# Kernel tuning notes

Measured on AMD Instinct MI355X. Metric: run time of the kernel, lower is better.

## Reference

```python
import jax, jax.numpy as jnp
import numpy as np

N_NODES = 50000
N_EDGES = 1_600_000
IN_DIM = 128
OUT_DIM = 32
HEADS = 4
EDGE_DIM = 16


def setup_inputs() -> dict:
    key = jax.random.key(0)
    ks = jax.random.split(key, 8)
    x = jax.random.normal(ks[0], (N_NODES, IN_DIM), dtype=jnp.float32)
    edge_index = jax.random.randint(ks[1], (2, N_EDGES), 0, N_NODES, dtype=jnp.int32)
    edge_attr = jax.random.normal(ks[2], (N_EDGES, EDGE_DIM), dtype=jnp.float32)
    # parameters (xavier-ish small scale)
    W_lin = jax.random.normal(ks[3], (OUT_DIM * HEADS, IN_DIM), dtype=jnp.float32) * 0.08
    att_src = jax.random.normal(ks[4], (HEADS, OUT_DIM), dtype=jnp.float32) * 0.1
    att_dst = jax.random.normal(ks[5], (HEADS, OUT_DIM), dtype=jnp.float32) * 0.1
    bias = jnp.zeros((OUT_DIM,), dtype=jnp.float32)
    W_edge = jax.random.normal(ks[6], (HEADS, EDGE_DIM), dtype=jnp.float32) * 0.2
    return {"x": x, "edge_index": edge_index, "edge_attr": edge_attr,
            "W_lin": W_lin, "att_src": att_src, "att_dst": att_dst,
            "bias": bias, "W_edge": W_edge}


def reference(x, edge_index, edge_attr, W_lin, att_src, att_dst, bias, W_edge):
    num_nodes = x.shape[0]
    heads, out_dim = att_src.shape
    # h = lin(x) -> [N, H, D]
    h = (x @ W_lin.T).reshape(num_nodes, heads, out_dim)
    # per-node attention terms [N, H]
    a_src = jnp.einsum("nhd,hd->nh", h, att_src)
    a_dst = jnp.einsum("nhd,hd->nh", h, att_dst)
    src, dst = edge_index[0], edge_index[1]
    # edge logits [E, H]
    logits = a_src[src] + a_dst[dst] + edge_attr @ W_edge.T
    logits = jax.nn.leaky_relu(logits, negative_slope=0.2)
    # segment softmax over edges grouped by dst (vectorized across heads)
    max_vals = jax.ops.segment_max(logits, dst, num_segments=num_nodes)  # [N, H]
    exp_s = jnp.exp(logits - max_vals[dst])
    denom = jax.ops.segment_sum(exp_s, dst, num_segments=num_nodes)  # [N, H]
    alpha = exp_s / (denom[dst] + 1e-16)  # [E, H]
    # weighted aggregation: sum_e h[src_e] * alpha_e into dst nodes
    out = h[src] * alpha[:, :, None]  # [E, H, D]
    agg = jax.ops.segment_sum(out, dst, num_segments=num_nodes)  # [N, H, D]
    return agg.mean(axis=1) + bias
```

## Files before the change

kernel.cpp:

```cpp
#include <hip/hip_runtime.h>
#include <hip/hip_fp16.h>

#define N_NODES 50000
#define N_EDGES 1600000
#define IN_DIM  128
#define OUT_DIM 32
#define HEADS   4
#define EDGE_DIM 16

#define NB   512
#define DPB  98
#define CAP  4096
#define SC_CHUNK 2048
#define SC_THREADS 512
#define SC_EPT   4

__global__ __launch_bounds__(256) void k_gemm(
    const float* __restrict__ x, const float* __restrict__ Wl,
    const float* __restrict__ att_src, const float* __restrict__ att_dst,
    __half* __restrict__ h2t, float* __restrict__ a_src,
    float* __restrict__ a_dst) {
  __shared__ float Wt[IN_DIM][68];
  __shared__ float xs[32][132];
  __shared__ float attS[IN_DIM], attD[IN_DIM];
  __shared__ float sred_s[32][4], sred_d[32][4];
  const int t = threadIdx.x;
  const int n0 = blockIdx.x * 32;

  if (t < IN_DIM) { attS[t] = att_src[t]; attD[t] = att_dst[t]; }

  for (int it = 0; it < 16; ++it) {
    int idx = it * 256 + t;
    int node = idx >> 7, i = idx & 127;
    int n = n0 + node;
    xs[node][i] = (n < N_NODES) ? x[(size_t)n * IN_DIM + i] : 0.f;
  }

  const int tx = t & 15, ty = t >> 4;
  const int na = n0 + 2 * ty, nb = na + 1;

  for (int p = 0; p < 2; ++p) {
    __syncthreads();
    for (int it = 0; it < 32; ++it) {
      int idx = it * 256 + t;
      int kg = (idx >> 7) + p * 64, i = idx & 127;
      Wt[i][kg - p * 64] = Wl[(size_t)kg * IN_DIM + i];
    }
    __syncthreads();

    float4 acc0 = {0.f,0.f,0.f,0.f}, acc1 = {0.f,0.f,0.f,0.f};
    for (int i4 = 0; i4 < IN_DIM; i4 += 4) {
      float4 xa = *(const float4*)&xs[2*ty][i4];
      float4 xb = *(const float4*)&xs[2*ty+1][i4];
      const float* xap = (const float*)&xa;
      const float* xbp = (const float*)&xb;
      #pragma unroll
      for (int ii = 0; ii < 4; ++ii) {
        float4 wv = *(const float4*)&Wt[i4+ii][tx*4];
        float a = xap[ii], b = xbp[ii];
        acc0.x += a*wv.x; acc0.y += a*wv.y; acc0.z += a*wv.z; acc0.w += a*wv.w;
        acc1.x += b*wv.x; acc1.y += b*wv.y; acc1.z += b*wv.z; acc1.w += b*wv.w;
      }
    }
    const int k = p*64 + tx*4;
    const int hd = k >> 5, d0 = k & 31;
    const float* ap = (const float*)&acc0;
    const float* bp = (const float*)&acc1;

    float sa = ap[0]*attS[k] + ap[1]*attS[k+1] + ap[2]*attS[k+2] + ap[3]*attS[k+3];
    float da = ap[0]*attD[k] + ap[1]*attD[k+1] + ap[2]*attD[k+2] + ap[3]*attD[k+3];
    float sb = bp[0]*attS[k] + bp[1]*attS[k+1] + bp[2]*attS[k+2] + bp[3]*attS[k+3];
    float db = bp[0]*attD[k] + bp[1]*attD[k+1] + bp[2]*attD[k+2] + bp[3]*attD[k+3];
    #pragma unroll
    for (int off = 1; off <= 4; off <<= 1) {
      sa += __shfl_xor(sa, off); da += __shfl_xor(da, off);
      sb += __shfl_xor(sb, off); db += __shfl_xor(db, off);
    }
    if ((tx & 7) == 0) {
      sred_s[2*ty][hd] = sa; sred_s[2*ty+1][hd] = sb;
      sred_d[2*ty][hd] = da; sred_d[2*ty+1][hd] = db;
    }

    if (na < N_NODES) {
      #pragma unroll
      for (int j = 0; j < 4; ++j)
        h2t[(size_t)na*IN_DIM + (d0+j)*4 + hd] = __float2half(ap[j]);
    }
    if (nb < N_NODES) {
      #pragma unroll
      for (int j = 0; j < 4; ++j)
        h2t[(size_t)nb*IN_DIM + (d0+j)*4 + hd] = __float2half(bp[j]);
    }
  }
  __syncthreads();
  if (t < 128) {
    int node = t >> 2;
    if (n0 + node < N_NODES)
      a_src[(size_t)(n0 + node) * 4 + (t & 3)] = sred_s[node][t & 3];
  } else {
    int tt = t - 128, node = tt >> 2;
    if (n0 + node < N_NODES)
      a_dst[(size_t)(n0 + node) * 4 + (tt & 3)] = sred_d[node][tt & 3];
  }
}

__global__ __launch_bounds__(SC_THREADS) void k_scatter2(
    const int* __restrict__ ei, const float* __restrict__ eattr,
    const float* __restrict__ a_src, const float* __restrict__ a_dst,
    const float* __restrict__ W_edge, unsigned int* __restrict__ gcursor,
    float4* __restrict__ rec, unsigned char* __restrict__ rdl) {
  __shared__ float We[HEADS * EDGE_DIM];
  __shared__ unsigned int cntb[NB], offb[NB];
  __shared__ float4 stg[SC_CHUNK];
  const int t = threadIdx.x;
  if (t < HEADS * EDGE_DIM) We[t] = W_edge[t];
  for (int i = t; i < NB; i += SC_THREADS) cntb[i] = 0u;
  __syncthreads();

  const int base = blockIdx.x * SC_CHUNK;
  unsigned int rx[SC_EPT], ry[SC_EPT], rz[SC_EPT], rw[SC_EPT], rk[SC_EPT];
  int bk[SC_EPT]; bool ok[SC_EPT];

  #pragma unroll
  for (int i = 0; i < SC_EPT; ++i) {
    int e = base + i * SC_THREADS + t;
    ok[i] = (e < N_EDGES);
    if (ok[i]) {
      int src = ei[e], dst = ei[N_EDGES + e];
      float asp[4], adp[4], ea[EDGE_DIM];
      *(float4*)asp = *(const float4*)(a_src + (size_t)src * 4);
      *(float4*)adp = *(const float4*)(a_dst + (size_t)dst * 4);
      #pragma unroll
      for (int j = 0; j < 4; ++j)
        *(float4*)&ea[j*4] = *(const float4*)(eattr + (size_t)e * EDGE_DIM + j*4);
      float pv[HEADS];
      #pragma unroll
      for (int hh = 0; hh < HEADS; ++hh) {
        float sum = asp[hh] + adp[hh];
        #pragma unroll
        for (int j = 0; j < EDGE_DIM; ++j) sum += ea[j] * We[hh*EDGE_DIM + j];
        float lg = (sum > 0.f) ? sum : 0.2f * sum;
        pv[hh] = __expf(lg);
      }
      __half2 p01 = __floats2half2_rn(pv[0], pv[1]);
      __half2 p23 = __floats2half2_rn(pv[2], pv[3]);
      int b = dst / DPB;
      bk[i] = b;
      rx[i] = *(const unsigned int*)&p01;
      ry[i] = *(const unsigned int*)&p23;
      rz[i] = (unsigned int)src;
      rw[i] = (unsigned int)(dst - b * DPB);
      rk[i] = atomicAdd(&cntb[b], 1u);
    }
  }
  __syncthreads();

  if (t < 64) {
    int carry = 0;
    for (int seg = 0; seg < 8; ++seg) {
      int v = (int)cntb[seg * 64 + t];
      int inc = v;
      #pragma unroll
      for (int off = 1; off < 64; off <<= 1) {
        int u = __shfl_up(inc, off);
        if (t >= off) inc += u;
      }
      offb[seg * 64 + t] = (unsigned int)(carry + inc - v);
      carry += __shfl(inc, 63);
    }
  }
  __syncthreads();

  #pragma unroll
  for (int i = 0; i < SC_EPT; ++i) {
    if (ok[i]) {
      float4 r;
      r.x = __uint_as_float(rx[i]); r.y = __uint_as_float(ry[i]);
      r.z = __uint_as_float(rz[i]); r.w = __uint_as_float(rw[i]);
      stg[offb[bk[i]] + rk[i]] = r;
    }
  }
  __syncthreads();

  {
    unsigned int c = cntb[t];
    if (c) {
      unsigned int gb = atomicAdd(&gcursor[t], c);
      unsigned int lo = offb[t];
      float4* dstp = rec + (size_t)t * CAP + gb;
      unsigned char* dl8 = rdl + (size_t)t * CAP + gb;
      for (unsigned int r = 0; r < c; ++r) {
        float4 v = stg[lo + r];
        dstp[r] = v;
        dl8[r] = (unsigned char)__float_as_uint(v.w);
      }
    }
  }
}

__global__ __launch_bounds__(1024) void k_bagg(
    const unsigned int* __restrict__ gcursor, const float4* __restrict__ rec,
    const unsigned char* __restrict__ rdl, const __half* __restrict__ h2t,
    const float* __restrict__ bias, float* __restrict__ out) {
  __shared__ unsigned short idx[CAP];
  __shared__ unsigned int cnt[DPB], off[DPB], cnt2[DPB];
  const int t = threadIdx.x;
  const int b = blockIdx.x;
  const size_t base = (size_t)b * CAP;
  const unsigned int cntT = gcursor[b];

  for (int i = t; i < DPB; i += 1024) { cnt[i] = 0u; cnt2[i] = 0u; }
  __syncthreads();

  for (unsigned int j = t; j < cntT; j += 1024)
    atomicAdd(&cnt[rdl[base + j]], 1u);
  __syncthreads();
  if (t == 0) {
    unsigned int run = 0;
    for (int i = 0; i < DPB; ++i) { off[i] = run; run += cnt[i]; }
  }
  __syncthreads();
  for (unsigned int j = t; j < cntT; j += 1024) {
    int dl = rdl[base + j];
    unsigned int r = atomicAdd(&cnt2[dl], 1u);
    idx[off[dl] + r] = (unsigned short)j;
  }
  __syncthreads();

  const int wv = t >> 6, lane = t & 63, half_ = lane >> 5, dd = lane & 31;
  for (int dl = wv; dl < DPB; dl += 16) {
    int node = b * DPB + dl;
    if (node >= N_NODES) break;
    const unsigned int s0 = off[dl], c = cnt[dl];

    float acc0 = 0.f, acc1 = 0.f, acc2 = 0.f, acc3 = 0.f;
    float dn0 = 0.f, dn1 = 0.f, dn2 = 0.f, dn3 = 0.f;

    unsigned int j = half_;
    for (; j + 2 < c; j += 4) {
      float4 ra = rec[base + idx[s0 + j]];
      float4 rb = rec[base + idx[s0 + j + 2]];
      unsigned int a01 = __float_as_uint(ra.x), a23 = __float_as_uint(ra.y);
      unsigned int b01 = __float_as_uint(rb.x), b23 = __float_as_uint(rb.y);
      int sa = (int)__float_as_uint(ra.z), sb = (int)__float_as_uint(rb.z);
      uint2 hra = *(const uint2*)(h2t + (size_t)sa * IN_DIM + dd * 4);
      uint2 hrb = *(const uint2*)(h2t + (size_t)sb * IN_DIM + dd * 4);
      float2 pa01 = __half22float2(*(const __half2*)&a01);
      float2 pa23 = __half22float2(*(const __half2*)&a23);
      dn0 += pa01.x; dn1 += pa01.y; dn2 += pa23.x; dn3 += pa23.y;
      float2 ha01 = __half22float2(*(const __half2*)&hra.x);
      float2 ha23 = __half22float2(*(const __half2*)&hra.y);
      acc0 += pa01.x * ha01.x; acc1 += pa01.y * ha01.y;
      acc2 += pa23.x * ha23.x; acc3 += pa23.y * ha23.y;
      float2 pb01 = __half22float2(*(const __half2*)&b01);
      float2 pb23 = __half22float2(*(const __half2*)&b23);
      dn0 += pb01.x; dn1 += pb01.y; dn2 += pb23.x; dn3 += pb23.y;
      float2 hb01 = __half22float2(*(const __half2*)&hrb.x);
      float2 hb23 = __half22float2(*(const __half2*)&hrb.y);
      acc0 += pb01.x * hb01.x; acc1 += pb01.y * hb01.y;
      acc2 += pb23.x * hb23.x; acc3 += pb23.y * hb23.y;
    }
    for (; j < c; j += 2) {
      float4 r = rec[base + idx[s0 + j]];
      unsigned int u01 = __float_as_uint(r.x), u23 = __float_as_uint(r.y);
      int src = (int)__float_as_uint(r.z);
      uint2 raw = *(const uint2*)(h2t + (size_t)src * IN_DIM + dd * 4);
      float2 p01 = __half22float2(*(const __half2*)&u01);
      float2 p23 = __half22float2(*(const __half2*)&u23);
      dn0 += p01.x; dn1 += p01.y; dn2 += p23.x; dn3 += p23.y;
      float2 h01 = __half22float2(*(const __half2*)&raw.x);
      float2 h23 = __half22float2(*(const __half2*)&raw.y);
      acc0 += p01.x * h01.x; acc1 += p01.y * h01.y;
      acc2 += p23.x * h23.x; acc3 += p23.y * h23.y;
    }

    dn0 += __shfl_xor(dn0, 32); dn1 += __shfl_xor(dn1, 32);
    dn2 += __shfl_xor(dn2, 32); dn3 += __shfl_xor(dn3, 32);
    acc0 += __shfl_xor(acc0, 32); acc1 += __shfl_xor(acc1, 32);
    acc2 += __shfl_xor(acc2, 32); acc3 += __shfl_xor(acc3, 32);

    if (half_ == 0) {
      float v = acc0 * (0.25f / (dn0 + 1e-16f)) + acc1 * (0.25f / (dn1 + 1e-16f))
              + acc2 * (0.25f / (dn2 + 1e-16f)) + acc3 * (0.25f / (dn3 + 1e-16f));
      out[(size_t)node * OUT_DIM + dd] = v + bias[dd];
    }
  }
}

extern "C" void kernel_launch(void* const* d_in, const int* in_sizes, int n_in,
                              void* d_out, int out_size, void* d_ws, size_t ws_size,
                              hipStream_t stream) {
  const float* x       = (const float*)d_in[0];
  const int*   ei      = (const int*)d_in[1];
  const float* eattr   = (const float*)d_in[2];
  const float* W_lin   = (const float*)d_in[3];
  const float* att_src = (const float*)d_in[4];
  const float* att_dst = (const float*)d_in[5];
  const float* bias    = (const float*)d_in[6];
  const float* W_edge  = (const float*)d_in[7];
  float* out = (float*)d_out;

  __half* h2t  = (__half*)d_ws;
  float4* rec  = (float4*)(h2t + (size_t)N_NODES * IN_DIM);
  unsigned char* rdl = (unsigned char*)(rec + (size_t)NB * CAP);
  float* a_src = (float*)(rdl + (size_t)NB * CAP);
  float* a_dst = a_src + (size_t)N_NODES * HEADS;
  unsigned int* gcursor = (unsigned int*)(a_dst + (size_t)N_NODES * HEADS);

  hipMemsetAsync(gcursor, 0, NB * sizeof(unsigned int), stream);

  k_gemm<<<(N_NODES + 31) / 32, 256, 0, stream>>>(
      x, W_lin, att_src, att_dst, h2t, a_src, a_dst);
  k_scatter2<<<(N_EDGES + SC_CHUNK - 1) / SC_CHUNK, SC_THREADS, 0, stream>>>(
      ei, eattr, a_src, a_dst, W_edge, gcursor, rec, rdl);
  k_bagg<<<NB, 1024, 0, stream>>>(gcursor, rec, rdl, h2t, bias, out);
}
```

Before: 193.3 us.

## Split edge scatter into separate logit-compute and bucketing kernels

The fused scatter kernel is split in two. A compute kernel writes per-edge exp-logits, src and dst as float4 records to a new intermediate buffer, and a bucketing kernel reads those records back, counts them into destination buckets in shared memory and writes the bucketed records. The aim is to lower register pressure and raise occupancy in each stage, so the gather-heavy compute and the shared-memory bucketing can each run at a better configuration. In exchange it adds an extra 25.6 MB write and read of the intermediate records plus one more kernel launch.

```diff
diff --git a/kernel.cpp b/kernel.cpp
--- a/kernel.cpp
+++ b/kernel.cpp
@@ -11,9 +11,8 @@
 #define NB   512
 #define DPB  98
 #define CAP  4096
-#define SC_CHUNK 2048
-#define SC_THREADS 512
-#define SC_EPT   4
+#define BK_CHUNK 2048
+#define BK_EPT   8
 
 __global__ __launch_bounds__(256) void k_gemm(
     const float* __restrict__ x, const float* __restrict__ Wl,
@@ -104,52 +103,67 @@
   }
 }
 
-__global__ __launch_bounds__(SC_THREADS) void k_scatter2(
+__global__ __launch_bounds__(256) void k_pcomp(
     const int* __restrict__ ei, const float* __restrict__ eattr,
     const float* __restrict__ a_src, const float* __restrict__ a_dst,
-    const float* __restrict__ W_edge, unsigned int* __restrict__ gcursor,
+    const float* __restrict__ W_edge, float4* __restrict__ rec1) {
+  __shared__ float We[HEADS * EDGE_DIM];
+  if (threadIdx.x < HEADS * EDGE_DIM) We[threadIdx.x] = W_edge[threadIdx.x];
+  __syncthreads();
+
+  const int base = blockIdx.x * 1024;
+  for (int k = 0; k < 4; ++k) {
+    int e = base + k * 256 + threadIdx.x;
+    if (e >= N_EDGES) break;
+    int src = ei[e], dst = ei[N_EDGES + e];
+    float asp[4], adp[4], ea[EDGE_DIM];
+    *(float4*)asp = *(const float4*)(a_src + (size_t)src * 4);
+    *(float4*)adp = *(const float4*)(a_dst + (size_t)dst * 4);
+    #pragma unroll
+    for (int j = 0; j < 4; ++j)
+      *(float4*)&ea[j*4] = *(const float4*)(eattr + (size_t)e * EDGE_DIM + j*4);
+    float pv[HEADS];
+    #pragma unroll
+    for (int hh = 0; hh < HEADS; ++hh) {
+      float sum = asp[hh] + adp[hh];
+      #pragma unroll
+      for (int j = 0; j < EDGE_DIM; ++j) sum += ea[j] * We[hh*EDGE_DIM + j];
+      float lg = (sum > 0.f) ? sum : 0.2f * sum;
+      pv[hh] = __expf(lg);
+    }
+    __half2 p01 = __floats2half2_rn(pv[0], pv[1]);
+    __half2 p23 = __floats2half2_rn(pv[2], pv[3]);
+    float4 r;
+    r.x = __uint_as_float(*(const unsigned int*)&p01);
+    r.y = __uint_as_float(*(const unsigned int*)&p23);
+    r.z = __uint_as_float((unsigned int)src);
+    r.w = __uint_as_float((unsigned int)dst);
+    rec1[e] = r;
+  }
+}
+
+__global__ __launch_bounds__(256) void k_bucket(
+    const float4* __restrict__ rec1, unsigned int* __restrict__ gcursor,
     float4* __restrict__ rec, unsigned char* __restrict__ rdl) {
-  __shared__ float We[HEADS * EDGE_DIM];
   __shared__ unsigned int cntb[NB], offb[NB];
-  __shared__ float4 stg[SC_CHUNK];
+  __shared__ float4 stg[BK_CHUNK];
   const int t = threadIdx.x;
-  if (t < HEADS * EDGE_DIM) We[t] = W_edge[t];
-  for (int i = t; i < NB; i += SC_THREADS) cntb[i] = 0u;
-  __syncthreads();
-
-  const int base = blockIdx.x * SC_CHUNK;
-  unsigned int rx[SC_EPT], ry[SC_EPT], rz[SC_EPT], rw[SC_EPT], rk[SC_EPT];
-  int bk[SC_EPT]; bool ok[SC_EPT];
+  for (int i = t; i < NB; i += 256) cntb[i] = 0u;
+  __syncthreads();
+
+  const int base = blockIdx.x * BK_CHUNK;
+  float4 r[BK_EPT]; unsigned int rk[BK_EPT]; int bk[BK_EPT]; bool ok[BK_EPT];
 
   #pragma unroll
-  for (int i = 0; i < SC_EPT; ++i) {
-    int e = base + i * SC_THREADS + t;
+  for (int i = 0; i < BK_EPT; ++i) {
+    int e = base + i * 256 + t;
     ok[i] = (e < N_EDGES);
     if (ok[i]) {
-      int src = ei[e], dst = ei[N_EDGES + e];
-      float asp[4], adp[4], ea[EDGE_DIM];
-      *(float4*)asp = *(const float4*)(a_src + (size_t)src * 4);
-      *(float4*)adp = *(const float4*)(a_dst + (size_t)dst * 4);
-      #pragma unroll
-      for (int j = 0; j < 4; ++j)
-        *(float4*)&ea[j*4] = *(const float4*)(eattr + (size_t)e * EDGE_DIM + j*4);
-      float pv[HEADS];
-      #pragma unroll
-      for (int hh = 0; hh < HEADS; ++hh) {
-        float sum = asp[hh] + adp[hh];
-        #pragma unroll
-        for (int j = 0; j < EDGE_DIM; ++j) sum += ea[j] * We[hh*EDGE_DIM + j];
-        float lg = (sum > 0.f) ? sum : 0.2f * sum;
-        pv[hh] = __expf(lg);
-      }
-      __half2 p01 = __floats2half2_rn(pv[0], pv[1]);
-      __half2 p23 = __floats2half2_rn(pv[2], pv[3]);
+      r[i] = rec1[e];
+      int dst = (int)__float_as_uint(r[i].w);
       int b = dst / DPB;
       bk[i] = b;
-      rx[i] = *(const unsigned int*)&p01;
-      ry[i] = *(const unsigned int*)&p23;
-      rz[i] = (unsigned int)src;
-      rw[i] = (unsigned int)(dst - b * DPB);
+      r[i].w = __uint_as_float((unsigned int)(dst - b * DPB));
       rk[i] = atomicAdd(&cntb[b], 1u);
     }
   }
@@ -172,27 +186,21 @@
   __syncthreads();
 
   #pragma unroll
-  for (int i = 0; i < SC_EPT; ++i) {
-    if (ok[i]) {
-      float4 r;
-      r.x = __uint_as_float(rx[i]); r.y = __uint_as_float(ry[i]);
-      r.z = __uint_as_float(rz[i]); r.w = __uint_as_float(rw[i]);
-      stg[offb[bk[i]] + rk[i]] = r;
-    }
-  }
-  __syncthreads();
-
-  {
-    unsigned int c = cntb[t];
+  for (int i = 0; i < BK_EPT; ++i)
+    if (ok[i]) stg[offb[bk[i]] + rk[i]] = r[i];
+  __syncthreads();
+
+  for (int b = t; b < NB; b += 256) {
+    unsigned int c = cntb[b];
     if (c) {
-      unsigned int gb = atomicAdd(&gcursor[t], c);
-      unsigned int lo = offb[t];
-      float4* dstp = rec + (size_t)t * CAP + gb;
-      unsigned char* dl8 = rdl + (size_t)t * CAP + gb;
-      for (unsigned int r = 0; r < c; ++r) {
-        float4 v = stg[lo + r];
-        dstp[r] = v;
-        dl8[r] = (unsigned char)__float_as_uint(v.w);
+      unsigned int gb = atomicAdd(&gcursor[b], c);
+      unsigned int lo = offb[b];
+      float4* dstp = rec + (size_t)b * CAP + gb;
+      unsigned char* dl8 = rdl + (size_t)b * CAP + gb;
+      for (unsigned int rr = 0; rr < c; ++rr) {
+        float4 v = stg[lo + rr];
+        dstp[rr] = v;
+        dl8[rr] = (unsigned char)__float_as_uint(v.w);
       }
     }
   }
@@ -302,7 +310,8 @@
 
   __half* h2t  = (__half*)d_ws;
   float4* rec  = (float4*)(h2t + (size_t)N_NODES * IN_DIM);
-  unsigned char* rdl = (unsigned char*)(rec + (size_t)NB * CAP);
+  float4* rec1 = rec + (size_t)NB * CAP;
+  unsigned char* rdl = (unsigned char*)(rec1 + (size_t)N_EDGES);
   float* a_src = (float*)(rdl + (size_t)NB * CAP);
   float* a_dst = a_src + (size_t)N_NODES * HEADS;
   unsigned int* gcursor = (unsigned int*)(a_dst + (size_t)N_NODES * HEADS);
@@ -311,7 +320,9 @@
 
   k_gemm<<<(N_NODES + 31) / 32, 256, 0, stream>>>(
       x, W_lin, att_src, att_dst, h2t, a_src, a_dst);
-  k_scatter2<<<(N_EDGES + SC_CHUNK - 1) / SC_CHUNK, SC_THREADS, 0, stream>>>(
-      ei, eattr, a_src, a_dst, W_edge, gcursor, rec, rdl);
+  k_pcomp<<<(N_EDGES + 1023) / 1024, 256, 0, stream>>>(
+      ei, eattr, a_src, a_dst, W_edge, rec1);
+  k_bucket<<<(N_EDGES + BK_CHUNK - 1) / BK_CHUNK, 256, 0, stream>>>(
+      rec1, gcursor, rec, rdl);
   k_bagg<<<NB, 1024, 0, stream>>>(gcursor, rec, rdl, h2t, bias, out);
 }
```

Measured after the change: 217.6 us. 12.6% more time.

## Scatter edge records directly to global bins, dropping shared-memory staging and scan

Applied to the files above, without the earlier changes.

The scatter kernel no longer runs a block-wide prefix scan or stages records in a 32KB shared buffer. Each bin now reserves its global range with one atomic, and each thread writes its float4 record and byte straight to that position. The block shrinks to 256 threads with 8 edges per thread. This removes LDS traffic, a barrier and the serial per-bin copy loop, and raises occupancy through lower shared-memory use. The cost is scattered, uncoalesced global writes in place of contiguous per-bin runs.

```diff
diff --git a/kernel.cpp b/kernel.cpp
--- a/kernel.cpp
+++ b/kernel.cpp
@@ -12,8 +12,7 @@
 #define DPB  98
 #define CAP  4096
 #define SC_CHUNK 2048
-#define SC_THREADS 512
-#define SC_EPT   4
+#define SC_EPT   8
 
 __global__ __launch_bounds__(256) void k_gemm(
     const float* __restrict__ x, const float* __restrict__ Wl,
@@ -104,26 +103,25 @@
   }
 }
 
-__global__ __launch_bounds__(SC_THREADS) void k_scatter2(
+__global__ __launch_bounds__(256) void k_scatter3(
     const int* __restrict__ ei, const float* __restrict__ eattr,
     const float* __restrict__ a_src, const float* __restrict__ a_dst,
     const float* __restrict__ W_edge, unsigned int* __restrict__ gcursor,
     float4* __restrict__ rec, unsigned char* __restrict__ rdl) {
   __shared__ float We[HEADS * EDGE_DIM];
-  __shared__ unsigned int cntb[NB], offb[NB];
-  __shared__ float4 stg[SC_CHUNK];
+  __shared__ unsigned int cntb[NB], gbase[NB];
   const int t = threadIdx.x;
   if (t < HEADS * EDGE_DIM) We[t] = W_edge[t];
-  for (int i = t; i < NB; i += SC_THREADS) cntb[i] = 0u;
+  for (int i = t; i < NB; i += 256) cntb[i] = 0u;
   __syncthreads();
 
   const int base = blockIdx.x * SC_CHUNK;
-  unsigned int rx[SC_EPT], ry[SC_EPT], rz[SC_EPT], rw[SC_EPT], rk[SC_EPT];
-  int bk[SC_EPT]; bool ok[SC_EPT];
+  unsigned int rx[SC_EPT], ry[SC_EPT], rz[SC_EPT], rk[SC_EPT];
+  int bk[SC_EPT]; unsigned char dl8[SC_EPT]; bool ok[SC_EPT];
 
   #pragma unroll
   for (int i = 0; i < SC_EPT; ++i) {
-    int e = base + i * SC_THREADS + t;
+    int e = base + i * 256 + t;
     ok[i] = (e < N_EDGES);
     if (ok[i]) {
       int src = ei[e], dst = ei[N_EDGES + e];
@@ -146,54 +144,28 @@
       __half2 p23 = __floats2half2_rn(pv[2], pv[3]);
       int b = dst / DPB;
       bk[i] = b;
+      dl8[i] = (unsigned char)(dst - b * DPB);
       rx[i] = *(const unsigned int*)&p01;
       ry[i] = *(const unsigned int*)&p23;
       rz[i] = (unsigned int)src;
-      rw[i] = (unsigned int)(dst - b * DPB);
       rk[i] = atomicAdd(&cntb[b], 1u);
     }
   }
   __syncthreads();
 
-  if (t < 64) {
-    int carry = 0;
-    for (int seg = 0; seg < 8; ++seg) {
-      int v = (int)cntb[seg * 64 + t];
-      int inc = v;
-      #pragma unroll
-      for (int off = 1; off < 64; off <<= 1) {
-        int u = __shfl_up(inc, off);
-        if (t >= off) inc += u;
-      }
-      offb[seg * 64 + t] = (unsigned int)(carry + inc - v);
-      carry += __shfl(inc, 63);
-    }
-  }
+  for (int b = t; b < NB; b += 256)
+    if (cntb[b]) gbase[b] = atomicAdd(&gcursor[b], cntb[b]);
   __syncthreads();
 
   #pragma unroll
   for (int i = 0; i < SC_EPT; ++i) {
     if (ok[i]) {
+      unsigned int pos = gbase[bk[i]] + rk[i];
       float4 r;
       r.x = __uint_as_float(rx[i]); r.y = __uint_as_float(ry[i]);
-      r.z = __uint_as_float(rz[i]); r.w = __uint_as_float(rw[i]);
-      stg[offb[bk[i]] + rk[i]] = r;
-    }
-  }
-  __syncthreads();
-
-  {
-    unsigned int c = cntb[t];
-    if (c) {
-      unsigned int gb = atomicAdd(&gcursor[t], c);
-      unsigned int lo = offb[t];
-      float4* dstp = rec + (size_t)t * CAP + gb;
-      unsigned char* dl8 = rdl + (size_t)t * CAP + gb;
-      for (unsigned int r = 0; r < c; ++r) {
-        float4 v = stg[lo + r];
-        dstp[r] = v;
-        dl8[r] = (unsigned char)__float_as_uint(v.w);
-      }
+      r.z = __uint_as_float(rz[i]); r.w = __uint_as_float((unsigned int)dl8[i]);
+      rec[(size_t)bk[i] * CAP + pos] = r;
+      rdl[(size_t)bk[i] * CAP + pos] = dl8[i];
     }
   }
 }
@@ -311,7 +283,7 @@
 
   k_gemm<<<(N_NODES + 31) / 32, 256, 0, stream>>>(
       x, W_lin, att_src, att_dst, h2t, a_src, a_dst);
-  k_scatter2<<<(N_EDGES + SC_CHUNK - 1) / SC_CHUNK, SC_THREADS, 0, stream>>>(
+  k_scatter3<<<(N_EDGES + SC_CHUNK - 1) / SC_CHUNK, 256, 0, stream>>>(
       ei, eattr, a_src, a_dst, W_edge, gcursor, rec, rdl);
   k_bagg<<<NB, 1024, 0, stream>>>(gcursor, rec, rdl, h2t, bias, out);
 }
```

Result: faster. 186.2 us (-3.7%).
